# Performance work log

Hardware: AMD Instinct MI355X
Metric: run time of the kernel (lower is better)

## Reference

```python
import jax, jax.numpy as jnp
import numpy as np

NX = 65536   # spatial cells
T = 32       # time points
H = 128      # MLP hidden width
DX = 1.0     # spatial resolution (init kwarg dx)
S0, S1 = -1.0, 1.0  # fixed stencil (learn_stencil=False)


def setup_inputs() -> dict:
    key = jax.random.key(0)
    k1, k2, k3, k4 = jax.random.split(key, 4)
    t = jnp.arange(T, dtype=jnp.float32) * 0.01          # time grid, dt=0.01
    u0 = jax.random.uniform(k1, (NX,), jnp.float32)      # initial state
    inv_sqrt_h = jnp.float32(1.0 / np.sqrt(H))
    W1 = jax.random.normal(k2, (1, H), jnp.float32)
    W2 = jax.random.normal(k3, (H, H), jnp.float32) * inv_sqrt_h
    W3 = jax.random.normal(k4, (H, 1), jnp.float32) * inv_sqrt_h
    D = jnp.full((1,), 0.01, jnp.float32)                # diffusion coefficient
    BC = jnp.zeros((2, 1), jnp.float32)                  # Dirichlet BC values
    return {"t": t, "u0": u0, "W1": W1, "W2": W2, "W3": W3, "D": D, "BC": BC}


def _flux(u, W1, W2, W3, D, BC):
    # per-cell MLP (func_nn): Linear->Tanh->Linear->Tanh->Linear, no bias, no sigmoid
    h = jnp.tanh(u[:, None] @ W1)        # [Nx, H]
    h = jnp.tanh(h @ W2)                 # [Nx, H]
    a = (h @ W3)[:, 0]                   # [Nx]
    a_plus = jax.nn.relu(a)
    a_min = -jax.nn.relu(-a)
    d = D[0]
    # left fluxes
    lb = d * (S0 * u[0] + S1 * BC[0, 0]) - a_plus[0] / DX * (-S0 * u[0] - S1 * BC[0, 0])
    ln = d * (S0 * u[1:] + S1 * u[:-1]) - a_plus[1:] / DX * (-S0 * u[1:] - S1 * u[:-1])
    left = jnp.concatenate([lb[None], ln])
    # right fluxes
    rb = d * (S0 * u[-1] + S1 * BC[1, 0]) - a_min[-1] / DX * (S0 * u[-1] + S1 * BC[1, 0])
    rn = d * (S0 * u[:-1] + S1 * u[1:]) - a_min[:-1] / DX * (S0 * u[:-1] + S1 * u[1:])
    right = jnp.concatenate([rn, rb[None]])
    return left + right


def reference(t, u0, W1, W2, W3, D, BC):
    # Neural-ODE integration of du/dt = flux_kernel(u); fixed-step RK4 over grid t
    f = lambda u: _flux(u, W1, W2, W3, D, BC)

    def step(u, dt):
        k1 = f(u)
        k2 = f(u + 0.5 * dt * k1)
        k3 = f(u + 0.5 * dt * k2)
        k4 = f(u + dt * k3)
        un = u + (dt / 6.0) * (k1 + 2.0 * k2 + 2.0 * k3 + k4)
        return un, un

    _, us = jax.lax.scan(step, u0, jnp.diff(t))
    return jnp.concatenate([u0[None], us], axis=0)  # [T, Nx]
```

## Files before the change

### kernel.cpp

```cpp
#include <hip/hip_runtime.h>

#define NXC 65536
#define TT 32
#define HH 128
#define BLK 256
#define HALO 124
#define WIN (BLK + 2 * HALO)
#define TABN 12289
#define TABLO (-2.5f)
#define TABINV 2048.0f

typedef __attribute__((ext_vector_type(8))) short bf16x8;
typedef __attribute__((ext_vector_type(4))) float f32x4;
typedef unsigned short u16;

__device__ __forceinline__ float bf2f(u16 b) {
    union { unsigned int u; float f; } v; v.u = ((unsigned int)b) << 16; return v.f;
}
__device__ __forceinline__ u16 f2bf(float f) {
    union { float f; unsigned int u; } v; v.f = f;
    return (u16)((v.u + 0x7fffu + ((v.u >> 16) & 1u)) >> 16);
}
__device__ __forceinline__ bool is_bf16_mode(const void* t) {
    return ((const u16*)t)[1] != 0;
}

#if __has_builtin(__builtin_amdgcn_exp2f)
#define EXP2F(x) __builtin_amdgcn_exp2f(x)
#else
#define EXP2F(x) exp2f(x)
#endif
#if __has_builtin(__builtin_amdgcn_rcpf)
#define RCPF(x) __builtin_amdgcn_rcpf(x)
#else
#define RCPF(x) (1.0f / (x))
#endif

__device__ __forceinline__ float fast_tanh(float x) {
    float e = EXP2F(x * 2.8853900817779268f);
    return 1.0f - 2.0f * RCPF(e + 1.0f);
}

__global__ void prep_kernel(const void* t, const void* W1, const void* W3,
                            const void* D, const void* BC, float* t32,
                            float* w1c, float* w3c, float* misc) {
    bool bf = is_bf16_mode(t);
    int tid = threadIdx.x;
    if (tid < TT)
        t32[tid] = bf ? bf2f(((const u16*)t)[tid]) : ((const float*)t)[tid];
    if (tid < HH) {
        w1c[tid] = bf ? bf2f(((const u16*)W1)[tid]) : ((const float*)W1)[tid];
        w3c[tid] = bf ? bf2f(((const u16*)W3)[tid]) : ((const float*)W3)[tid];
    }
    if (tid == 0) {
        misc[0] = bf ? bf2f(((const u16*)D)[0]) : ((const float*)D)[0];
        misc[1] = bf ? bf2f(((const u16*)BC)[0]) : ((const float*)BC)[0];
        misc[2] = bf ? bf2f(((const u16*)BC)[1]) : ((const float*)BC)[1];
    }
}

__global__ void u0cvt_kernel(const void* t, const void* u0,
                             float* __restrict__ u, void* out) {
    bool bf = is_bf16_mode(t);
    int i = blockIdx.x * 256 + threadIdx.x;
    if (bf) {
        u16 v = ((const u16*)u0)[i];
        u[i] = bf2f(v);
        ((u16*)out)[i] = v;
    } else {
        float v = ((const float*)u0)[i];
        u[i] = v;
        ((float*)out)[i] = v;
    }
}

__global__ void w2swz_kernel(const void* t, const void* W2,
                             u16* __restrict__ w2frag) {
    bool bf = is_bf16_mode(t);
    int i = blockIdx.x * 256 + threadIdx.x;
    int j = i & 7;
    int lane = (i >> 3) & 63;
    int ks = (i >> 9) & 3;
    int nt = i >> 11;
    int k = ks * 32 + (lane >> 4) * 8 + j;
    int n = nt * 16 + (lane & 15);
    w2frag[i] = bf ? ((const u16*)W2)[k * HH + n]
                   : f2bf(((const float*)W2)[k * HH + n]);
}

__global__ __launch_bounds__(256) void tabbuild_kernel(
    const float* __restrict__ w1c, const float* __restrict__ w3c,
    const u16* __restrict__ w2frag, float* __restrict__ atab) {
    __shared__ float w1s[HH];
    __shared__ float w3s[HH];
    int tid = threadIdx.x;
    if (tid < HH) w1s[tid] = w1c[tid];
    else          w3s[tid - HH] = w3c[tid - HH];
    __syncthreads();

    int lane = tid & 63;
    int wave = tid >> 6;
    int q = lane >> 4;
    int m = lane & 15;
    int base = (blockIdx.x * 4 + wave) * 16;
    float uin = TABLO + (float)(base + m) * (1.0f / TABINV);

    bf16x8 afrag[4];
#pragma unroll
    for (int ks = 0; ks < 4; ++ks)
#pragma unroll
        for (int j = 0; j < 8; ++j) {
            float h = fast_tanh(uin * w1s[ks * 32 + q * 8 + j]);
            afrag[ks][j] = (short)f2bf(h);
        }

    const bf16x8* w2f = (const bf16x8*)w2frag;
    float p0 = 0.f, p1 = 0.f, p2 = 0.f, p3 = 0.f;
#pragma unroll
    for (int nt = 0; nt < 8; ++nt) {
        f32x4 acc = {0.f, 0.f, 0.f, 0.f};
#pragma unroll
        for (int ks = 0; ks < 4; ++ks) {
            bf16x8 b = w2f[(nt * 4 + ks) * 64 + lane];
            acc = __builtin_amdgcn_mfma_f32_16x16x32_bf16(afrag[ks], b, acc, 0, 0, 0);
        }
        float w3v = w3s[nt * 16 + m];
        p0 += fast_tanh(acc[0]) * w3v;
        p1 += fast_tanh(acc[1]) * w3v;
        p2 += fast_tanh(acc[2]) * w3v;
        p3 += fast_tanh(acc[3]) * w3v;
    }
#pragma unroll
    for (int sh = 1; sh < 16; sh <<= 1) {
        p0 += __shfl_xor(p0, sh, 64);
        p1 += __shfl_xor(p1, sh, 64);
        p2 += __shfl_xor(p2, sh, 64);
        p3 += __shfl_xor(p3, sh, 64);
    }
    int r = m & 3;
    float a = (r == 0) ? p0 : (r == 1) ? p1 : (r == 2) ? p2 : p3;
    if (m < 4) {
        int e = base + q * 4 + r;
        if (e < TABN) atab[e] = a;
    }
}

__global__ __launch_bounds__(256) void fused_kernel(
    const float* __restrict__ u32, const float* __restrict__ t32,
    const float* __restrict__ misc, const float* __restrict__ atab,
    void* outbase, const void* traw) {
    __shared__ float tab[TABN + 1];
    __shared__ float vs[2][WIN];

    int t = threadIdx.x;
    int b = blockIdx.x;
    for (int i = t; i < TABN; i += BLK) tab[i] = atab[i];

    int gbase = b * BLK - HALO;
    float d = misc[0], bc0 = misc[1], bc1 = misc[2];
    bool bf = is_bf16_mode(traw);

    float ub[2], vso[2], kacc[2], k[2];
    bool gok[2], isl[2], isr[2];
#pragma unroll
    for (int j = 0; j < 2; ++j) {
        int i = t + j * BLK;
        int g = gbase + i;
        bool inw = (i < WIN);
        bool ok = inw && (g >= 0) && (g < NXC);
        gok[j] = ok;
        float v = ok ? u32[g] : 0.0f;
        ub[j] = v;
        vso[j] = v;
        if (inw) vs[0][i] = v;
        isl[j] = (g == 0);
        isr[j] = (g == NXC - 1);
    }
    int ownj = (t >= HALO) ? 0 : 1;
    int owng = gbase + t + ownj * 0 + ((t >= HALO) ? 0 : BLK);
    __syncthreads();

    int cur = 0;
    for (int step = 0; step < TT - 1; ++step) {
        float dt = t32[step + 1] - t32[step];
        float dt2 = 0.5f * dt, dt6 = dt * (1.0f / 6.0f);
        kacc[0] = 0.f;
        kacc[1] = 0.f;
#pragma unroll
        for (int s = 0; s < 4; ++s) {
            int sigma = step * 4 + s;
            float cnext = (s < 2) ? dt2 : dt;
            float w = (s == 1 || s == 2) ? 2.f : 1.f;
#pragma unroll
            for (int j = 0; j < 2; ++j) {
                int i = t + j * BLK;
                bool act = gok[j] && (i > sigma) && (i < WIN - 1 - sigma);
                float kk = 0.f;
                if (act) {
                    float vc = vso[j];
                    float vl = isl[j] ? bc0 : vs[cur][i - 1];
                    float vr = isr[j] ? bc1 : vs[cur][i + 1];
                    float f = fmaf(vc, TABINV, -TABLO * TABINV);
                    f = fminf(fmaxf(f, 0.0f), (float)(TABN - 1));
                    int i0 = (int)f;
                    i0 = min(i0, TABN - 2);
                    float frac = f - (float)i0;
                    float t0 = tab[i0], t1 = tab[i0 + 1];
                    float a = fmaf(frac, t1 - t0, t0);
                    float ap = fmaxf(a, 0.f);
                    float am = fminf(a, 0.f);
                    kk = (vl - vc) * (d + ap) + (vr - vc) * (d - am);
                }
                k[j] = kk;
                kacc[j] += w * kk;
            }
#pragma unroll
            for (int j = 0; j < 2; ++j) {
                int i = t + j * BLK;
                bool act = gok[j] && (i > sigma) && (i < WIN - 1 - sigma);
                if (act) {
                    float vn;
                    if (s < 3) {
                        vn = fmaf(cnext, k[j], ub[j]);
                    } else {
                        vn = fmaf(dt6, kacc[j], ub[j]);
                        ub[j] = vn;
                    }
                    vso[j] = vn;
                    vs[cur ^ 1][i] = vn;
                }
            }
            cur ^= 1;
            __syncthreads();
        }
        float uo = ub[ownj];
        if (bf) ((u16*)outbase)[(size_t)(step + 1) * NXC + owng] = f2bf(uo);
        else    ((float*)outbase)[(size_t)(step + 1) * NXC + owng] = uo;
    }
}

extern "C" void kernel_launch(void* const* d_in, const int* in_sizes, int n_in,
                              void* d_out, int out_size, void* d_ws,
                              size_t ws_size, hipStream_t stream) {
    const void* t  = d_in[0];
    const void* u0 = d_in[1];
    const void* W1 = d_in[2];
    const void* W2 = d_in[3];
    const void* W3 = d_in[4];
    const void* Dp = d_in[5];
    const void* BC = d_in[6];

    float* u_a  = (float*)d_ws;
    float* t32  = u_a + NXC;
    float* w1c  = t32 + TT;
    float* w3c  = w1c + HH;
    float* misc = w3c + HH;
    float* atab = misc + 4;
    u16* w2frag = (u16*)(atab + TABN + 3);

    prep_kernel<<<1, 256, 0, stream>>>(t, W1, W3, Dp, BC, t32, w1c, w3c, misc);
    w2swz_kernel<<<64, 256, 0, stream>>>(t, W2, w2frag);
    u0cvt_kernel<<<NXC / 256, 256, 0, stream>>>(t, u0, u_a, d_out);
    tabbuild_kernel<<<(TABN + 63) / 64, 256, 0, stream>>>(w1c, w3c, w2frag, atab);
    fused_kernel<<<NXC / BLK, 256, 0, stream>>>(u_a, t32, misc, atab, d_out, t);
}
```

Baseline: 121.4 us.

## Make each wave own an independent halo window, exchanging neighbours with shuffles

```diff
diff --git a/kernel.cpp b/kernel.cpp
--- a/kernel.cpp
+++ b/kernel.cpp
@@ -3,12 +3,12 @@
 #define NXC 65536
 #define TT 32
 #define HH 128
-#define BLK 256
-#define HALO 124
-#define WIN (BLK + 2 * HALO)
 #define TABN 12289
 #define TABLO (-2.5f)
 #define TABINV 2048.0f
+#define OUTW 64
+#define VC 5
+#define WINW 320
 
 typedef __attribute__((ext_vector_type(8))) short bf16x8;
 typedef __attribute__((ext_vector_type(4))) float f32x4;
@@ -39,39 +39,6 @@
 __device__ __forceinline__ float fast_tanh(float x) {
     float e = EXP2F(x * 2.8853900817779268f);
     return 1.0f - 2.0f * RCPF(e + 1.0f);
-}
-
-__global__ void prep_kernel(const void* t, const void* W1, const void* W3,
-                            const void* D, const void* BC, float* t32,
-                            float* w1c, float* w3c, float* misc) {
-    bool bf = is_bf16_mode(t);
-    int tid = threadIdx.x;
-    if (tid < TT)
-        t32[tid] = bf ? bf2f(((const u16*)t)[tid]) : ((const float*)t)[tid];
-    if (tid < HH) {
-        w1c[tid] = bf ? bf2f(((const u16*)W1)[tid]) : ((const float*)W1)[tid];
-        w3c[tid] = bf ? bf2f(((const u16*)W3)[tid]) : ((const float*)W3)[tid];
-    }
-    if (tid == 0) {
-        misc[0] = bf ? bf2f(((const u16*)D)[0]) : ((const float*)D)[0];
-        misc[1] = bf ? bf2f(((const u16*)BC)[0]) : ((const float*)BC)[0];
-        misc[2] = bf ? bf2f(((const u16*)BC)[1]) : ((const float*)BC)[1];
-    }
-}
-
-__global__ void u0cvt_kernel(const void* t, const void* u0,
-                             float* __restrict__ u, void* out) {
-    bool bf = is_bf16_mode(t);
-    int i = blockIdx.x * 256 + threadIdx.x;
-    if (bf) {
-        u16 v = ((const u16*)u0)[i];
-        u[i] = bf2f(v);
-        ((u16*)out)[i] = v;
-    } else {
-        float v = ((const float*)u0)[i];
-        u[i] = v;
-        ((float*)out)[i] = v;
-    }
 }
 
 __global__ void w2swz_kernel(const void* t, const void* W2,
@@ -89,13 +56,17 @@
 }
 
 __global__ __launch_bounds__(256) void tabbuild_kernel(
-    const float* __restrict__ w1c, const float* __restrict__ w3c,
+    const void* traw, const void* W1, const void* W3,
     const u16* __restrict__ w2frag, float* __restrict__ atab) {
     __shared__ float w1s[HH];
     __shared__ float w3s[HH];
+    bool bf = is_bf16_mode(traw);
     int tid = threadIdx.x;
-    if (tid < HH) w1s[tid] = w1c[tid];
-    else          w3s[tid - HH] = w3c[tid - HH];
+    if (tid < HH)
+        w1s[tid] = bf ? bf2f(((const u16*)W1)[tid]) : ((const float*)W1)[tid];
+    else
+        w3s[tid - HH] = bf ? bf2f(((const u16*)W3)[tid - HH])
+                           : ((const float*)W3)[tid - HH];
     __syncthreads();
 
     int lane = tid & 63;
@@ -146,96 +117,107 @@
 }
 
 __global__ __launch_bounds__(256) void fused_kernel(
-    const float* __restrict__ u32, const float* __restrict__ t32,
-    const float* __restrict__ misc, const float* __restrict__ atab,
-    void* outbase, const void* traw) {
-    __shared__ float tab[TABN + 1];
-    __shared__ float vs[2][WIN];
-
-    int t = threadIdx.x;
-    int b = blockIdx.x;
-    for (int i = t; i < TABN; i += BLK) tab[i] = atab[i];
-
-    int gbase = b * BLK - HALO;
-    float d = misc[0], bc0 = misc[1], bc1 = misc[2];
+    const void* traw, const void* u0raw, const void* Draw, const void* BCraw,
+    const float* __restrict__ atab, void* outbase) {
+    __shared__ float tab[TABN];
+    __shared__ float t32s[TT];
+
+    int tid = threadIdx.x;
     bool bf = is_bf16_mode(traw);
-
-    float ub[2], vso[2], kacc[2], k[2];
-    bool gok[2], isl[2], isr[2];
-#pragma unroll
-    for (int j = 0; j < 2; ++j) {
-        int i = t + j * BLK;
-        int g = gbase + i;
-        bool inw = (i < WIN);
-        bool ok = inw && (g >= 0) && (g < NXC);
-        gok[j] = ok;
-        float v = ok ? u32[g] : 0.0f;
-        ub[j] = v;
-        vso[j] = v;
-        if (inw) vs[0][i] = v;
+    for (int i = tid; i < TABN; i += 256) tab[i] = atab[i];
+    if (tid < TT)
+        t32s[tid] = bf ? bf2f(((const u16*)traw)[tid]) : ((const float*)traw)[tid];
+
+    float d   = bf ? bf2f(((const u16*)Draw)[0])  : ((const float*)Draw)[0];
+    float bc0 = bf ? bf2f(((const u16*)BCraw)[0]) : ((const float*)BCraw)[0];
+    float bc1 = bf ? bf2f(((const u16*)BCraw)[1]) : ((const float*)BCraw)[1];
+
+    int lane = tid & 63;
+    int wid = blockIdx.x * 4 + (tid >> 6);
+    int o0 = wid * OUTW;
+    int wsg = o0 - 128;
+    int gb = wsg + lane * VC;
+    int i0 = lane * VC;
+
+    float v[VC], ub[VC], kacc[VC], kk[VC];
+    bool gok[VC], isl[VC], isr[VC], own[VC];
+#pragma unroll
+    for (int j = 0; j < VC; ++j) {
+        int g = gb + j;
+        int i = i0 + j;
+        gok[j] = (g >= 0) && (g < NXC);
         isl[j] = (g == 0);
         isr[j] = (g == NXC - 1);
-    }
-    int ownj = (t >= HALO) ? 0 : 1;
-    int owng = gbase + t + ownj * 0 + ((t >= HALO) ? 0 : BLK);
+        own[j] = (i >= 128) && (i < 128 + OUTW);
+        float x = 0.f;
+        if (gok[j])
+            x = bf ? bf2f(((const u16*)u0raw)[g]) : ((const float*)u0raw)[g];
+        v[j] = x;
+        ub[j] = x;
+        if (own[j]) {
+            if (bf) ((u16*)outbase)[g] = f2bf(x);
+            else    ((float*)outbase)[g] = x;
+        }
+    }
     __syncthreads();
 
-    int cur = 0;
     for (int step = 0; step < TT - 1; ++step) {
-        float dt = t32[step + 1] - t32[step];
+        float dt = t32s[step + 1] - t32s[step];
         float dt2 = 0.5f * dt, dt6 = dt * (1.0f / 6.0f);
-        kacc[0] = 0.f;
-        kacc[1] = 0.f;
+#pragma unroll
+        for (int j = 0; j < VC; ++j) kacc[j] = 0.f;
 #pragma unroll
         for (int s = 0; s < 4; ++s) {
             int sigma = step * 4 + s;
             float cnext = (s < 2) ? dt2 : dt;
-            float w = (s == 1 || s == 2) ? 2.f : 1.f;
-#pragma unroll
-            for (int j = 0; j < 2; ++j) {
-                int i = t + j * BLK;
-                bool act = gok[j] && (i > sigma) && (i < WIN - 1 - sigma);
-                float kk = 0.f;
+            float wgt = (s == 1 || s == 2) ? 2.f : 1.f;
+            float vup = __shfl_up(v[VC - 1], 1, 64);
+            float vdn = __shfl_down(v[0], 1, 64);
+#pragma unroll
+            for (int j = 0; j < VC; ++j) {
+                float vc = v[j];
+                float vl = (j == 0) ? vup : v[j - 1];
+                float vr = (j == VC - 1) ? vdn : v[j + 1];
+                vl = isl[j] ? bc0 : vl;
+                vr = isr[j] ? bc1 : vr;
+                float f = fmaf(vc, TABINV, (-TABLO) * TABINV);
+                f = fminf(fmaxf(f, 0.0f), (float)(TABN - 1));
+                int e0 = (int)f;
+                e0 = min(e0, TABN - 2);
+                float frac = f - (float)e0;
+                float t0 = tab[e0], t1 = tab[e0 + 1];
+                float a = fmaf(frac, t1 - t0, t0);
+                float ap = fmaxf(a, 0.f);
+                float am = fminf(a, 0.f);
+                float kv = (vl - vc) * (d + ap) + (vr - vc) * (d - am);
+                int i = i0 + j;
+                bool act = gok[j] && (i > sigma) && (i < WINW - 1 - sigma);
+                kk[j] = act ? kv : 0.f;
+            }
+#pragma unroll
+            for (int j = 0; j < VC; ++j) {
+                int i = i0 + j;
+                bool act = gok[j] && (i > sigma) && (i < WINW - 1 - sigma);
+                kacc[j] += wgt * kk[j];
                 if (act) {
-                    float vc = vso[j];
-                    float vl = isl[j] ? bc0 : vs[cur][i - 1];
-                    float vr = isr[j] ? bc1 : vs[cur][i + 1];
-                    float f = fmaf(vc, TABINV, -TABLO * TABINV);
-                    f = fminf(fmaxf(f, 0.0f), (float)(TABN - 1));
-                    int i0 = (int)f;
-                    i0 = min(i0, TABN - 2);
-                    float frac = f - (float)i0;
-                    float t0 = tab[i0], t1 = tab[i0 + 1];
-                    float a = fmaf(frac, t1 - t0, t0);
-                    float ap = fmaxf(a, 0.f);
-                    float am = fminf(a, 0.f);
-                    kk = (vl - vc) * (d + ap) + (vr - vc) * (d - am);
-                }
-                k[j] = kk;
-                kacc[j] += w * kk;
-            }
-#pragma unroll
-            for (int j = 0; j < 2; ++j) {
-                int i = t + j * BLK;
-                bool act = gok[j] && (i > sigma) && (i < WIN - 1 - sigma);
-                if (act) {
-                    float vn;
                     if (s < 3) {
-                        vn = fmaf(cnext, k[j], ub[j]);
+                        v[j] = fmaf(cnext, kk[j], ub[j]);
                     } else {
-                        vn = fmaf(dt6, kacc[j], ub[j]);
+                        float vn = fmaf(dt6, kacc[j], ub[j]);
+                        v[j] = vn;
                         ub[j] = vn;
                     }
-                    vso[j] = vn;
-                    vs[cur ^ 1][i] = vn;
                 }
             }
-            cur ^= 1;
-            __syncthreads();
-        }
-        float uo = ub[ownj];
-        if (bf) ((u16*)outbase)[(size_t)(step + 1) * NXC + owng] = f2bf(uo);
-        else    ((float*)outbase)[(size_t)(step + 1) * NXC + owng] = uo;
+        }
+        size_t rb = (size_t)(step + 1) * NXC;
+#pragma unroll
+        for (int j = 0; j < VC; ++j) {
+            if (own[j]) {
+                if (bf) ((u16*)outbase)[rb + gb + j] = f2bf(ub[j]);
+                else    ((float*)outbase)[rb + gb + j] = ub[j];
+            }
+        }
     }
 }
 
@@ -250,17 +232,10 @@
     const void* Dp = d_in[5];
     const void* BC = d_in[6];
 
-    float* u_a  = (float*)d_ws;
-    float* t32  = u_a + NXC;
-    float* w1c  = t32 + TT;
-    float* w3c  = w1c + HH;
-    float* misc = w3c + HH;
-    float* atab = misc + 4;
+    float* atab = (float*)d_ws;
     u16* w2frag = (u16*)(atab + TABN + 3);
 
-    prep_kernel<<<1, 256, 0, stream>>>(t, W1, W3, Dp, BC, t32, w1c, w3c, misc);
     w2swz_kernel<<<64, 256, 0, stream>>>(t, W2, w2frag);
-    u0cvt_kernel<<<NXC / 256, 256, 0, stream>>>(t, u0, u_a, d_out);
-    tabbuild_kernel<<<(TABN + 63) / 64, 256, 0, stream>>>(w1c, w3c, w2frag, atab);
-    fused_kernel<<<NXC / BLK, 256, 0, stream>>>(u_a, t32, misc, atab, d_out, t);
-}
+    tabbuild_kernel<<<(TABN + 63) / 64, 256, 0, stream>>>(t, W1, W3, w2frag, atab);
+    fused_kernel<<<NXC / (OUTW * 4), 256, 0, stream>>>(t, u0, Dp, BC, atab, d_out);
+}
```

New measurement: 127.7 us. +5.2%, slower.
